# Kernel tuning notes

Measured on AMD Instinct MI355X. Metric: run time of the kernel, lower is better.

The kernel has to match this reference:

```python
import jax, jax.numpy as jnp
import numpy as np

EPS = 1e-5
SCALE = 30.0

def _ln(x, g, b):
    m = jnp.mean(x, axis=-1, keepdims=True)
    v = jnp.mean((x - m) ** 2, axis=-1, keepdims=True)
    return (x - m) * jax.lax.rsqrt(v + EPS) * g + b

def setup_inputs() -> dict:
    key = jax.random.key(0)
    ks = jax.random.split(key, 12)
    B, L, K, H, NIN = 4, 2048, 48, 128, 512
    s = 0.02
    return {
        "h_V": jax.random.normal(ks[0], (B, L, H), jnp.float32),
        "h_E": jax.random.normal(ks[1], (B, L, K, NIN - H), jnp.float32),
        "mask_V": jnp.ones((B, L), jnp.float32),
        "mask_E": jnp.ones((B, L, K), jnp.float32),
        "w1": jax.random.normal(ks[2], (NIN, H), jnp.float32) * s,
        "b1": jnp.zeros((H,), jnp.float32),
        "w2": jax.random.normal(ks[3], (H, H), jnp.float32) * s,
        "b2": jnp.zeros((H,), jnp.float32),
        "w3": jax.random.normal(ks[4], (H, H), jnp.float32) * s,
        "b3": jnp.zeros((H,), jnp.float32),
        "g1": jnp.ones((H,), jnp.float32),
        "bn1": jnp.zeros((H,), jnp.float32),
        "g2": jnp.ones((H,), jnp.float32),
        "bn2": jnp.zeros((H,), jnp.float32),
        "wf1": jax.random.normal(ks[5], (H, 4 * H), jnp.float32) * s,
        "bf1": jnp.zeros((4 * H,), jnp.float32),
        "wf2": jax.random.normal(ks[6], (4 * H, H), jnp.float32) * s,
        "bf2": jnp.zeros((H,), jnp.float32),
    }

def reference(h_V, h_E, mask_V, mask_E, w1, b1, w2, b2, w3, b3, g1, bn1, g2, bn2, wf1, bf1, wf2, bf2):
    B, L, H = h_V.shape
    K = h_E.shape[-2]
    gelu = lambda x: jax.nn.gelu(x, approximate=False)  # torch nn.GELU default (erf)
    # expand source node over K neighbors and concat: (B,L,K,num_in)
    h_V_exp = jnp.broadcast_to(h_V[:, :, None, :], (B, L, K, H))
    h_EV = jnp.concatenate([h_V_exp, h_E], axis=-1)
    h_msg = gelu(jnp.einsum('blki,ih->blkh', h_EV, w1) + b1)
    h_msg = gelu(jnp.einsum('blkh,hj->blkj', h_msg, w2) + b2)
    h_msg = jnp.einsum('blkh,hj->blkj', h_msg, w3) + b3
    h_msg = mask_E[..., None] * h_msg
    dh = jnp.sum(h_msg, axis=-2) / SCALE  # masked sum-aggregate over K
    h = _ln(h_V + dh, g1, bn1)
    dff = jnp.einsum('blh,hf->blf', h, wf1) + bf1
    dff = jnp.einsum('blf,fh->blh', gelu(dff), wf2) + bf2
    h = _ln(h + dff, g2, bn2)
    return mask_V[..., None] * h
```

## Files before the change

kernel.cpp:

```cpp
#include <hip/hip_runtime.h>
#include <hip/hip_bf16.h>


typedef __bf16 bf16x8 __attribute__((ext_vector_type(8)));
typedef __bf16 bf16x4 __attribute__((ext_vector_type(4)));
typedef float f32x4 __attribute__((ext_vector_type(4)));

#define HH 128
#define EE 384
#define KK 48

__device__ __forceinline__ float gelu_f(float x) {
  float x2 = x * x;
  float u = x * (-1.5957691216f - 0.0713548163f * x2);
  float e = __expf(u);
  return __fdividef(x, 1.0f + e);
}

__device__ __forceinline__ bf16x8 cvt8v(f32x4 a, f32x4 b) {
  bf16x8 r;
  #pragma unroll
  for (int i = 0; i < 4; ++i) { r[i] = (__bf16)a[i]; r[i + 4] = (__bf16)b[i]; }
  return r;
}

__device__ __forceinline__ f32x4 mfma16(bf16x8 a, bf16x8 b, f32x4 c) {
  return __builtin_amdgcn_mfma_f32_16x16x32_bf16(a, b, c, 0, 0, 0);
}

__device__ __forceinline__ void gload16(const void* g, void* l) {
  __builtin_amdgcn_global_load_lds(
      (const __attribute__((address_space(1))) void*)g,
      (__attribute__((address_space(3))) void*)l, 16, 0, 0);
}

__global__ void prep_kernel(const float* __restrict__ w1, const float* __restrict__ w2,
                            const float* __restrict__ w3, const float* __restrict__ wf1,
                            const float* __restrict__ wf2, __bf16* __restrict__ out) {
  int idx = blockIdx.x * 256 + threadIdx.x;
  if (idx < 49152) {
    int t = idx & 7, lane = (idx >> 3) & 63, n = (idx >> 9) & 7, kc = idx >> 12;
    int e = kc * 32 + (lane >> 4) * 8 + t, h = n * 16 + (lane & 15);
    out[idx] = (__bf16)w1[(128 + e) * 128 + h];
  } else if (idx < 65536) {
    int u = idx - 49152;
    int t = u & 7, lane = (u >> 3) & 63, n = (u >> 9) & 7, kc = u >> 12;
    int e = kc * 32 + (lane >> 4) * 8 + t, h = n * 16 + (lane & 15);
    out[idx] = (__bf16)w2[e * 128 + h];
  } else if (idx < 81920) {
    int u = idx - 65536;
    int t = u & 7, lane = (u >> 3) & 63, n = (u >> 9) & 7, kc = u >> 12;
    int e = kc * 32 + (lane >> 4) * 8 + t, h = n * 16 + (lane & 15);
    out[idx] = (__bf16)w3[e * 128 + h];
  } else if (idx < 147456) {
    int t = idx - 81920; int f = t >> 7, h = t & 127;
    out[idx] = (__bf16)wf1[h * 512 + f];
  } else if (idx < 212992) {
    int t = idx - 147456; int h = t >> 9, f = t & 511;
    out[idx] = (__bf16)wf2[f * 128 + h];
  }
}

__global__ __launch_bounds__(128) void v1_kernel(const float* __restrict__ hV,
                                                 const float* __restrict__ w1,
                                                 const float* __restrict__ b1,
                                                 float* __restrict__ V1) {
  __shared__ __align__(16) float sV[16][128];
  const int tid = threadIdx.x;
  const long p0 = (long)blockIdx.x * 16;
  for (int i = 0; i < 16; ++i) sV[i][tid] = hV[(p0 + i) * HH + tid];
  __syncthreads();
  float acc[16];
  float bb = b1[tid];
  #pragma unroll
  for (int p = 0; p < 16; ++p) acc[p] = bb;
  for (int k = 0; k < 128; k += 4) {
    float wa = w1[(k + 0) * HH + tid];
    float wb = w1[(k + 1) * HH + tid];
    float wc = w1[(k + 2) * HH + tid];
    float wd = w1[(k + 3) * HH + tid];
    #pragma unroll
    for (int p = 0; p < 16; ++p) {
      float4 h4 = *(const float4*)&sV[p][k];
      acc[p] = fmaf(h4.x, wa, fmaf(h4.y, wb, fmaf(h4.z, wc, fmaf(h4.w, wd, acc[p]))));
    }
  }
  #pragma unroll
  for (int p = 0; p < 16; ++p) V1[(p0 + p) * HH + tid] = acc[p];
}

__global__ __launch_bounds__(256, 2) void msg_kernel(
    const float* __restrict__ hE, const float* __restrict__ hV,
    const float* __restrict__ maskE,
    const __bf16* __restrict__ w1f, const __bf16* __restrict__ w2f,
    const __bf16* __restrict__ w3f, const float* __restrict__ V1,
    const float* __restrict__ b2, const float* __restrict__ b3,
    const float* __restrict__ g1, const float* __restrict__ bn1,
    float* __restrict__ outH) {
  __shared__ __align__(16) float sStage[4][4608];

  const int tid = threadIdx.x;
  const int lane = tid & 63;
  const int w = tid >> 6;
  const long p = (long)blockIdx.x * 4 + w;
  const int fr = lane & 15;
  const int fg = lane >> 4;
  char* stDst = (char*)&sStage[w][0];
  const int swz = (fr & 7) << 4;

  const int r_l = lane >> 3;
  const int cswz = ((lane & 7) ^ r_l) * 16;
  const char* gA = (const char*)(hE + p * KK * (long)EE) + r_l * (EE * 4) + cswz;

  const __bf16* b1p = w1f + lane * 8;
  const __bf16* b2p = w2f + lane * 8;
  const __bf16* b3p = w3f + lane * 8;

  f32x4 acc[3][8];
  #pragma unroll
  for (int m = 0; m < 3; ++m)
    #pragma unroll
    for (int n = 0; n < 8; ++n) acc[m][n] = (f32x4){0.f, 0.f, 0.f, 0.f};

  bf16x8 BsA[8], BsB[8];

#define STAGEA(KC, BUFI) { \
    _Pragma("unroll") for (int q_ = 0; q_ < 6; ++q_) \
      gload16(gA + (KC) * 128 + q_ * (8 * EE * 4), stDst + (BUFI) * 6144 + q_ * 1024); }
#define LOADB(BUF, BP, KC) { \
    _Pragma("unroll") for (int n_ = 0; n_ < 8; ++n_) \
      BUF[n_] = *(const bf16x8*)((BP) + ((KC) * 8 + n_) * 512); }
#define WAITV(N) asm volatile("s_waitcnt vmcnt(" #N ")" ::: "memory")

#define GITER(WAITN, BUFI, BUSE, DOSTAGE, STKC, STBUF, DOB, BLP, BLKC) { \
    WAITV(WAITN); \
    const char* rb_ = stDst + (BUFI) * 6144; \
    f32x4 x0_ = *(const f32x4*)(rb_ + fr * 128 + ((fg * 32) ^ swz)); \
    f32x4 x1_ = *(const f32x4*)(rb_ + fr * 128 + ((fg * 32 + 16) ^ swz)); \
    f32x4 x2_ = *(const f32x4*)(rb_ + (16 + fr) * 128 + ((fg * 32) ^ swz)); \
    f32x4 x3_ = *(const f32x4*)(rb_ + (16 + fr) * 128 + ((fg * 32 + 16) ^ swz)); \
    f32x4 x4_ = *(const f32x4*)(rb_ + (32 + fr) * 128 + ((fg * 32) ^ swz)); \
    f32x4 x5_ = *(const f32x4*)(rb_ + (32 + fr) * 128 + ((fg * 32 + 16) ^ swz)); \
    if (DOSTAGE) STAGEA(STKC, STBUF); \
    bf16x8 af0 = cvt8v(x0_, x1_); \
    bf16x8 af1 = cvt8v(x2_, x3_); \
    bf16x8 af2 = cvt8v(x4_, x5_); \
    _Pragma("unroll") for (int n_ = 0; n_ < 8; ++n_) { \
      acc[0][n_] = mfma16(BUSE[n_], af0, acc[0][n_]); \
      acc[1][n_] = mfma16(BUSE[n_], af1, acc[1][n_]); \
      acc[2][n_] = mfma16(BUSE[n_], af2, acc[2][n_]); } \
    if (DOB) LOADB(BUSE, BLP, BLKC); }

#define STEPL(BUSE, KC, DOB, BLP, BLKC) { \
    const int cb_ = (((KC) * 64 + fg * 16) ^ swz); \
    bf16x8 af0 = *(const bf16x8*)(stDst + fr * 256 + cb_); \
    bf16x8 af1 = *(const bf16x8*)(stDst + (16 + fr) * 256 + cb_); \
    bf16x8 af2 = *(const bf16x8*)(stDst + (32 + fr) * 256 + cb_); \
    _Pragma("unroll") for (int n_ = 0; n_ < 8; ++n_) { \
      acc[0][n_] = mfma16(BUSE[n_], af0, acc[0][n_]); \
      acc[1][n_] = mfma16(BUSE[n_], af1, acc[1][n_]); \
      acc[2][n_] = mfma16(BUSE[n_], af2, acc[2][n_]); } \
    if (DOB) LOADB(BUSE, BLP, BLKC); }

#define EPI(BIASQ) { \
    _Pragma("unroll") for (int m_ = 0; m_ < 3; ++m_) { \
      const int rb_ = (m_ * 16 + fr) * 256; \
      _Pragma("unroll") for (int n_ = 0; n_ < 8; ++n_) { \
        bf16x4 t_; \
        _Pragma("unroll") for (int j_ = 0; j_ < 4; ++j_) \
          t_[j_] = (__bf16)gelu_f(acc[m_][n_][j_] + BIASQ[n_][j_]); \
        *(bf16x4*)(stDst + rb_ + ((n_ * 32 + fg * 8) ^ swz)) = t_; \
        acc[m_][n_] = (f32x4){0.f, 0.f, 0.f, 0.f}; } } }

  STAGEA(0, 0);
  LOADB(BsA, b1p, 0);
  STAGEA(1, 1);
  LOADB(BsB, b1p, 1);

  GITER(14, 0, BsA, 1, 2, 2, 1, b1p, 2);
  GITER(14, 1, BsB, 1, 3, 0, 1, b1p, 3);
  GITER(14, 2, BsA, 1, 4, 1, 1, b1p, 4);
  GITER(14, 0, BsB, 1, 5, 2, 1, b1p, 5);
  GITER(14, 1, BsA, 1, 6, 0, 1, b1p, 6);
  GITER(14, 2, BsB, 1, 7, 1, 1, b1p, 7);
  GITER(14, 0, BsA, 1, 8, 2, 1, b1p, 8);
  GITER(14, 1, BsB, 1, 9, 0, 1, b1p, 9);
  GITER(14, 2, BsA, 1, 10, 1, 1, b1p, 10);
  GITER(14, 0, BsB, 1, 11, 2, 1, b1p, 11);

  f32x4 vq[8];
  #pragma unroll
  for (int n = 0; n < 8; ++n) vq[n] = *(const f32x4*)(V1 + p * HH + n * 16 + fg * 4);

  GITER(22, 1, BsA, 0, 0, 0, 1, b2p, 0);
  GITER(16, 2, BsB, 0, 0, 0, 1, b2p, 1);

  EPI(vq);

  { WAITV(8);  STEPL(BsA, 0, 1, b2p, 2); }
  { WAITV(8);  STEPL(BsB, 1, 1, b2p, 3); }
  { WAITV(8);  STEPL(BsA, 2, 1, b3p, 0); }
  { WAITV(8);  STEPL(BsB, 3, 1, b3p, 1); }
  {
    f32x4 bq[8];
    #pragma unroll
    for (int n = 0; n < 8; ++n) bq[n] = *(const f32x4*)(b2 + n * 16 + fg * 4);
    EPI(bq);
  }

  { STEPL(BsA, 0, 1, b3p, 2); }
  { STEPL(BsB, 1, 1, b3p, 3); }
  { WAITV(8);  STEPL(BsA, 2, 0, b3p, 0); }
  { WAITV(0);  STEPL(BsB, 3, 0, b3p, 0); }

  const float mk0 = maskE[p * KK + fr];
  const float mk1 = maskE[p * KK + 16 + fr];
  const float mk2 = maskE[p * KK + 32 + fr];
  f32x4 red[8];
  {
    #pragma unroll
    for (int n = 0; n < 8; ++n) {
      f32x4 bq = *(const f32x4*)(b3 + n * 16 + fg * 4);
      red[n] = mk0 * (acc[0][n] + bq) + mk1 * (acc[1][n] + bq) + mk2 * (acc[2][n] + bq);
    }
    #pragma unroll
    for (int off = 1; off <= 8; off <<= 1)
      #pragma unroll
      for (int n = 0; n < 8; ++n)
        #pragma unroll
        for (int j = 0; j < 4; ++j)
          red[n][j] += __shfl_xor(red[n][j], off);
  }

  {
    f32x4 xq[8];
    #pragma unroll
    for (int n = 0; n < 8; ++n)
      xq[n] = *(const f32x4*)(hV + p * HH + n * 16 + fg * 4) + red[n] * (1.f / 30.f);
    float s = 0.f;
    #pragma unroll
    for (int n = 0; n < 8; ++n)
      #pragma unroll
      for (int j = 0; j < 4; ++j) s += xq[n][j];
    s += __shfl_xor(s, 16); s += __shfl_xor(s, 32);
    float mean = s * (1.f / 128.f);
    float qv = 0.f;
    #pragma unroll
    for (int n = 0; n < 8; ++n)
      #pragma unroll
      for (int j = 0; j < 4; ++j) { float e = xq[n][j] - mean; qv += e * e; }
    qv += __shfl_xor(qv, 16); qv += __shfl_xor(qv, 32);
    float rs = rsqrtf(qv * (1.f / 128.f) + 1e-5f);
    if (fr == 0) {
      #pragma unroll
      for (int n = 0; n < 8; ++n) {
        f32x4 gq = *(const f32x4*)(g1 + n * 16 + fg * 4);
        f32x4 bq = *(const f32x4*)(bn1 + n * 16 + fg * 4);
        f32x4 o;
        #pragma unroll
        for (int j = 0; j < 4; ++j) o[j] = (xq[n][j] - mean) * rs * gq[j] + bq[j];
        *(f32x4*)(outH + p * HH + n * 16 + fg * 4) = o;
      }
    }
  }
#undef STAGEA
#undef LOADB
#undef WAITV
#undef GITER
#undef STEPL
#undef EPI
}

__global__ __launch_bounds__(256, 2) void ffn_kernel(
    const float* __restrict__ xin, const __bf16* __restrict__ wf1t,
    const float* __restrict__ bf1, const __bf16* __restrict__ wf2t,
    const float* __restrict__ bf2, const float* __restrict__ g2,
    const float* __restrict__ bn2, const float* __restrict__ maskV,
    float* __restrict__ out) {
  __shared__ __align__(16) __bf16 sX[32][136];
  __shared__ __align__(16) __bf16 sH1[32][520];
  __shared__ __align__(16) float sOut[32][132];
  const int tid = threadIdx.x, lane = tid & 63, w = tid >> 6;
  const long row0 = (long)blockIdx.x * 32;
  const int fr = lane & 15, fg = lane >> 4;

  {
    int r = tid >> 3, c = (tid & 7) * 16;
    const float* src = xin + (row0 + r) * HH + c;
    f32x4 v0 = *(const f32x4*)src, v1 = *(const f32x4*)(src + 4);
    f32x4 v2 = *(const f32x4*)(src + 8), v3 = *(const f32x4*)(src + 12);
    *(bf16x8*)&sX[r][c] = cvt8v(v0, v1);
    *(bf16x8*)&sX[r][c + 8] = cvt8v(v2, v3);
  }
  __syncthreads();

  f32x4 a1[2][8];
  #pragma unroll
  for (int m = 0; m < 2; ++m)
    #pragma unroll
    for (int n = 0; n < 8; ++n) a1[m][n] = (f32x4){0.f, 0.f, 0.f, 0.f};
  for (int kc = 0; kc < 4; ++kc) {
    int k0 = kc * 32;
    bf16x8 af0 = *(const bf16x8*)&sX[fr][k0 + fg * 8];
    bf16x8 af1 = *(const bf16x8*)&sX[16 + fr][k0 + fg * 8];
    #pragma unroll
    for (int n = 0; n < 8; ++n) {
      const __bf16* bp = wf1t + (long)(w * 128 + n * 16 + fr) * HH + k0 + fg * 8;
      bf16x8 bfr = *(const bf16x8*)bp;
      a1[0][n] = mfma16(af0, bfr, a1[0][n]);
      a1[1][n] = mfma16(af1, bfr, a1[1][n]);
    }
  }
  #pragma unroll
  for (int n = 0; n < 8; ++n) {
    float bv = bf1[w * 128 + n * 16 + fr];
    #pragma unroll
    for (int m = 0; m < 2; ++m)
      #pragma unroll
      for (int j = 0; j < 4; ++j)
        sH1[m * 16 + fg * 4 + j][w * 128 + n * 16 + fr] = (__bf16)gelu_f(a1[m][n][j] + bv);
  }
  __syncthreads();

  f32x4 a2[2][2];
  #pragma unroll
  for (int m = 0; m < 2; ++m)
    #pragma unroll
    for (int n = 0; n < 2; ++n) a2[m][n] = (f32x4){0.f, 0.f, 0.f, 0.f};
  for (int kc = 0; kc < 16; ++kc) {
    int k0 = kc * 32;
    bf16x8 af0 = *(const bf16x8*)&sH1[fr][k0 + fg * 8];
    bf16x8 af1 = *(const bf16x8*)&sH1[16 + fr][k0 + fg * 8];
    #pragma unroll
    for (int n = 0; n < 2; ++n) {
      const __bf16* bp = wf2t + (long)(w * 32 + n * 16 + fr) * 512 + k0 + fg * 8;
      bf16x8 bfr = *(const bf16x8*)bp;
      a2[0][n] = mfma16(af0, bfr, a2[0][n]);
      a2[1][n] = mfma16(af1, bfr, a2[1][n]);
    }
  }
  #pragma unroll
  for (int n = 0; n < 2; ++n) {
    float bv = bf2[w * 32 + n * 16 + fr];
    #pragma unroll
    for (int m = 0; m < 2; ++m)
      #pragma unroll
      for (int j = 0; j < 4; ++j)
        sOut[m * 16 + fg * 4 + j][w * 32 + n * 16 + fr] = a2[m][n][j] + bv;
  }
  __syncthreads();

  {
    int r = tid >> 3, c0 = (tid & 7) * 16;
    long p = row0 + r;
    const float* xp = xin + p * HH + c0;
    float x[16];
    #pragma unroll
    for (int i = 0; i < 16; ++i) x[i] = xp[i] + sOut[r][c0 + i];
    float s = 0.f;
    #pragma unroll
    for (int i = 0; i < 16; ++i) s += x[i];
    s += __shfl_xor(s, 1); s += __shfl_xor(s, 2); s += __shfl_xor(s, 4);
    float mean = s * (1.f / 128.f);
    float q = 0.f;
    #pragma unroll
    for (int i = 0; i < 16; ++i) { float e = x[i] - mean; q += e * e; }
    q += __shfl_xor(q, 1); q += __shfl_xor(q, 2); q += __shfl_xor(q, 4);
    float rs = rsqrtf(q * (1.f / 128.f) + 1e-5f);
    float mv = maskV[p];
    float* op = out + p * HH + c0;
    #pragma unroll
    for (int i = 0; i < 16; ++i)
      op[i] = ((x[i] - mean) * rs * g2[c0 + i] + bn2[c0 + i]) * mv;
  }
}

extern "C" void kernel_launch(void* const* d_in, const int* in_sizes, int n_in,
                              void* d_out, int out_size, void* d_ws, size_t ws_size,
                              hipStream_t stream) {
  const float* hV    = (const float*)d_in[0];
  const float* hE    = (const float*)d_in[1];
  const float* maskV = (const float*)d_in[2];
  const float* maskE = (const float*)d_in[3];
  const float* w1    = (const float*)d_in[4];
  const float* b1    = (const float*)d_in[5];
  const float* w2    = (const float*)d_in[6];
  const float* b2    = (const float*)d_in[7];
  const float* w3    = (const float*)d_in[8];
  const float* b3    = (const float*)d_in[9];
  const float* g1    = (const float*)d_in[10];
  const float* bn1   = (const float*)d_in[11];
  const float* g2    = (const float*)d_in[12];
  const float* bn2   = (const float*)d_in[13];
  const float* wf1   = (const float*)d_in[14];
  const float* bf1   = (const float*)d_in[15];
  const float* wf2   = (const float*)d_in[16];
  const float* bf2   = (const float*)d_in[17];
  float* out = (float*)d_out;

  __bf16* wsb = (__bf16*)d_ws;
  float* V1   = (float*)((char*)d_ws + 425984);
  float* hbuf = (float*)((char*)d_ws + 4620288);

  prep_kernel<<<832, 256, 0, stream>>>(w1, w2, w3, wf1, wf2, wsb);
  v1_kernel<<<512, 128, 0, stream>>>(hV, w1, b1, V1);
  msg_kernel<<<2048, 256, 0, stream>>>(hE, hV, maskE,
                                       wsb, wsb + 49152, wsb + 65536, V1,
                                       b2, b3, g1, bn1, hbuf);
  ffn_kernel<<<256, 256, 0, stream>>>(hbuf, wsb + 81920, bf1, wsb + 147456, bf2,
                                      g2, bn2, maskV, out);
}
```

Baseline: 211.9 us.

## Process two nodes per wave in msg_kernel with cross-node prefetch pipelining

Each wave now handles two nodes instead of one, and the grid is halved. The first h_E chunks of the second node are prefetched into LDS during the first node's layer-2/3 work, so the second node's load latency hides behind compute. V1 and hV rows are staged into LDS through async global_load_lds, and the bias and LayerNorm parameters are cached in shared memory once per block. In exchange the kernel gets much more complex vmcnt accounting, uses more LDS per block, and launches half as many blocks, which gives fewer of them to spread across the GPU.

```diff
diff --git a/kernel.cpp b/kernel.cpp
--- a/kernel.cpp
+++ b/kernel.cpp
@@ -32,6 +32,11 @@
   __builtin_amdgcn_global_load_lds(
       (const __attribute__((address_space(1))) void*)g,
       (__attribute__((address_space(3))) void*)l, 16, 0, 0);
+}
+__device__ __forceinline__ void gload4(const void* g, void* l) {
+  __builtin_amdgcn_global_load_lds(
+      (const __attribute__((address_space(1))) void*)g,
+      (__attribute__((address_space(3))) void*)l, 4, 0, 0);
 }
 
 __global__ void prep_kernel(const float* __restrict__ w1, const float* __restrict__ w2,
@@ -98,24 +103,43 @@
     const float* __restrict__ g1, const float* __restrict__ bn1,
     float* __restrict__ outH) {
   __shared__ __align__(16) float sStage[4][4608];
+  __shared__ __align__(16) float sAux[4][256];
+  __shared__ __align__(16) float sBias[512];
 
   const int tid = threadIdx.x;
   const int lane = tid & 63;
   const int w = tid >> 6;
-  const long p = (long)blockIdx.x * 4 + w;
   const int fr = lane & 15;
   const int fg = lane >> 4;
+
+  for (int j = tid; j < 512; j += 256) {
+    float v;
+    if (j < 128) v = b2[j];
+    else if (j < 256) v = b3[j - 128];
+    else if (j < 384) v = g1[j - 256];
+    else v = bn1[j - 384];
+    sBias[j] = v;
+  }
+  __syncthreads();
+
+  const long p0 = (long)blockIdx.x * 8 + w * 2;
+  const long p1 = p0 + 1;
   char* stDst = (char*)&sStage[w][0];
+  char* auxDst = (char*)&sAux[w][0];
+  const char* biasB = (const char*)&sBias[0];
   const int swz = (fr & 7) << 4;
-
   const int r_l = lane >> 3;
   const int cswz = ((lane & 7) ^ r_l) * 16;
-  const char* gA = (const char*)(hE + p * KK * (long)EE) + r_l * (EE * 4) + cswz;
+  const char* gA0 = (const char*)(hE + p0 * KK * (long)EE) + r_l * (EE * 4) + cswz;
+  const char* gA1 = gA0 + (long)KK * EE * 4;
 
   const __bf16* b1p = w1f + lane * 8;
   const __bf16* b2p = w2f + lane * 8;
   const __bf16* b3p = w3f + lane * 8;
 
+  const float mkA0 = maskE[p0 * KK + fr], mkA1 = maskE[p0 * KK + 16 + fr], mkA2 = maskE[p0 * KK + 32 + fr];
+  const float mkB0 = maskE[p1 * KK + fr], mkB1 = maskE[p1 * KK + 16 + fr], mkB2 = maskE[p1 * KK + 32 + fr];
+
   f32x4 acc[3][8];
   #pragma unroll
   for (int m = 0; m < 3; ++m)
@@ -124,16 +148,21 @@
 
   bf16x8 BsA[8], BsB[8];
 
-#define STAGEA(KC, BUFI) { \
+#define STAGEA(GB, KC, BUFI) { \
     _Pragma("unroll") for (int q_ = 0; q_ < 6; ++q_) \
-      gload16(gA + (KC) * 128 + q_ * (8 * EE * 4), stDst + (BUFI) * 6144 + q_ * 1024); }
+      gload16((GB) + (KC) * 128 + q_ * (8 * EE * 4), stDst + (BUFI) * 6144 + q_ * 1024); }
+#define STAGEAUX(PP) { \
+    gload4(V1 + (PP) * HH + lane, auxDst); \
+    gload4(V1 + (PP) * HH + 64 + lane, auxDst + 256); \
+    gload4(hV + (PP) * HH + lane, auxDst + 512); \
+    gload4(hV + (PP) * HH + 64 + lane, auxDst + 768); }
 #define LOADB(BUF, BP, KC) { \
     _Pragma("unroll") for (int n_ = 0; n_ < 8; ++n_) \
       BUF[n_] = *(const bf16x8*)((BP) + ((KC) * 8 + n_) * 512); }
 #define WAITV(N) asm volatile("s_waitcnt vmcnt(" #N ")" ::: "memory")
 
-#define GITER(WAITN, BUFI, BUSE, DOSTAGE, STKC, STBUF, DOB, BLP, BLKC) { \
-    WAITV(WAITN); \
+#define GITER(WN, BUFI, BUSE, DOSTAGE, GB, STKC, STBUF, BLP, BLKC) { \
+    WAITV(WN); \
     const char* rb_ = stDst + (BUFI) * 6144; \
     f32x4 x0_ = *(const f32x4*)(rb_ + fr * 128 + ((fg * 32) ^ swz)); \
     f32x4 x1_ = *(const f32x4*)(rb_ + fr * 128 + ((fg * 32 + 16) ^ swz)); \
@@ -141,7 +170,7 @@
     f32x4 x3_ = *(const f32x4*)(rb_ + (16 + fr) * 128 + ((fg * 32 + 16) ^ swz)); \
     f32x4 x4_ = *(const f32x4*)(rb_ + (32 + fr) * 128 + ((fg * 32) ^ swz)); \
     f32x4 x5_ = *(const f32x4*)(rb_ + (32 + fr) * 128 + ((fg * 32 + 16) ^ swz)); \
-    if (DOSTAGE) STAGEA(STKC, STBUF); \
+    if (DOSTAGE) STAGEA(GB, STKC, STBUF); \
     bf16x8 af0 = cvt8v(x0_, x1_); \
     bf16x8 af1 = cvt8v(x2_, x3_); \
     bf16x8 af2 = cvt8v(x4_, x5_); \
@@ -149,9 +178,10 @@
       acc[0][n_] = mfma16(BUSE[n_], af0, acc[0][n_]); \
       acc[1][n_] = mfma16(BUSE[n_], af1, acc[1][n_]); \
       acc[2][n_] = mfma16(BUSE[n_], af2, acc[2][n_]); } \
-    if (DOB) LOADB(BUSE, BLP, BLKC); }
-
-#define STEPL(BUSE, KC, DOB, BLP, BLKC) { \
+    LOADB(BUSE, BLP, BLKC); }
+
+#define STEPL(WN, BUSE, KC, DOB, BLP, BLKC) { \
+    WAITV(WN); \
     const int cb_ = (((KC) * 64 + fg * 16) ^ swz); \
     bf16x8 af0 = *(const bf16x8*)(stDst + fr * 256 + cb_); \
     bf16x8 af1 = *(const bf16x8*)(stDst + (16 + fr) * 256 + cb_); \
@@ -162,113 +192,146 @@
       acc[2][n_] = mfma16(BUSE[n_], af2, acc[2][n_]); } \
     if (DOB) LOADB(BUSE, BLP, BLKC); }
 
-#define EPI(BIASQ) { \
+#define EPICORE(BQ) { \
     _Pragma("unroll") for (int m_ = 0; m_ < 3; ++m_) { \
       const int rb_ = (m_ * 16 + fr) * 256; \
       _Pragma("unroll") for (int n_ = 0; n_ < 8; ++n_) { \
         bf16x4 t_; \
         _Pragma("unroll") for (int j_ = 0; j_ < 4; ++j_) \
-          t_[j_] = (__bf16)gelu_f(acc[m_][n_][j_] + BIASQ[n_][j_]); \
+          t_[j_] = (__bf16)gelu_f(acc[m_][n_][j_] + BQ[n_][j_]); \
         *(bf16x4*)(stDst + rb_ + ((n_ * 32 + fg * 8) ^ swz)) = t_; \
         acc[m_][n_] = (f32x4){0.f, 0.f, 0.f, 0.f}; } } }
 
-  STAGEA(0, 0);
+#define REDLN(M0, M1, M2, PP) { \
+    f32x4 red[8]; \
+    _Pragma("unroll") for (int n_ = 0; n_ < 8; ++n_) { \
+      f32x4 bq_ = *(const f32x4*)(biasB + (128 + n_ * 16 + fg * 4) * 4); \
+      red[n_] = (M0) * (acc[0][n_] + bq_) + (M1) * (acc[1][n_] + bq_) + (M2) * (acc[2][n_] + bq_); \
+      acc[0][n_] = (f32x4){0.f, 0.f, 0.f, 0.f}; \
+      acc[1][n_] = (f32x4){0.f, 0.f, 0.f, 0.f}; \
+      acc[2][n_] = (f32x4){0.f, 0.f, 0.f, 0.f}; } \
+    _Pragma("unroll") for (int off_ = 1; off_ <= 8; off_ <<= 1) \
+      _Pragma("unroll") for (int n_ = 0; n_ < 8; ++n_) \
+        _Pragma("unroll") for (int j_ = 0; j_ < 4; ++j_) \
+          red[n_][j_] += __shfl_xor(red[n_][j_], off_); \
+    f32x4 xq[8]; \
+    _Pragma("unroll") for (int n_ = 0; n_ < 8; ++n_) { \
+      f32x4 hq_ = *(const f32x4*)(auxDst + 512 + (n_ * 16 + fg * 4) * 4); \
+      xq[n_] = hq_ + red[n_] * (1.f / 30.f); } \
+    float s_ = 0.f; \
+    _Pragma("unroll") for (int n_ = 0; n_ < 8; ++n_) \
+      _Pragma("unroll") for (int j_ = 0; j_ < 4; ++j_) s_ += xq[n_][j_]; \
+    s_ += __shfl_xor(s_, 16); s_ += __shfl_xor(s_, 32); \
+    float mean_ = s_ * (1.f / 128.f); \
+    float qv_ = 0.f; \
+    _Pragma("unroll") for (int n_ = 0; n_ < 8; ++n_) \
+      _Pragma("unroll") for (int j_ = 0; j_ < 4; ++j_) { float e_ = xq[n_][j_] - mean_; qv_ += e_ * e_; } \
+    qv_ += __shfl_xor(qv_, 16); qv_ += __shfl_xor(qv_, 32); \
+    float rs_ = rsqrtf(qv_ * (1.f / 128.f) + 1e-5f); \
+    if (fr == 0) { \
+      _Pragma("unroll") for (int n_ = 0; n_ < 8; ++n_) { \
+        f32x4 gq_ = *(const f32x4*)(biasB + (256 + n_ * 16 + fg * 4) * 4); \
+        f32x4 bq_ = *(const f32x4*)(biasB + (384 + n_ * 16 + fg * 4) * 4); \
+        f32x4 o_; \
+        _Pragma("unroll") for (int j_ = 0; j_ < 4; ++j_) \
+          o_[j_] = (xq[n_][j_] - mean_) * rs_ * gq_[j_] + bq_[j_]; \
+        *(f32x4*)(outH + (PP) * HH + n_ * 16 + fg * 4) = o_; } } }
+
+  STAGEA(gA0, 0, 0);
   LOADB(BsA, b1p, 0);
-  STAGEA(1, 1);
+  STAGEA(gA0, 1, 1);
   LOADB(BsB, b1p, 1);
 
-  GITER(14, 0, BsA, 1, 2, 2, 1, b1p, 2);
-  GITER(14, 1, BsB, 1, 3, 0, 1, b1p, 3);
-  GITER(14, 2, BsA, 1, 4, 1, 1, b1p, 4);
-  GITER(14, 0, BsB, 1, 5, 2, 1, b1p, 5);
-  GITER(14, 1, BsA, 1, 6, 0, 1, b1p, 6);
-  GITER(14, 2, BsB, 1, 7, 1, 1, b1p, 7);
-  GITER(14, 0, BsA, 1, 8, 2, 1, b1p, 8);
-  GITER(14, 1, BsB, 1, 9, 0, 1, b1p, 9);
-  GITER(14, 2, BsA, 1, 10, 1, 1, b1p, 10);
-  GITER(14, 0, BsB, 1, 11, 2, 1, b1p, 11);
-
-  f32x4 vq[8];
-  #pragma unroll
-  for (int n = 0; n < 8; ++n) vq[n] = *(const f32x4*)(V1 + p * HH + n * 16 + fg * 4);
-
-  GITER(22, 1, BsA, 0, 0, 0, 1, b2p, 0);
-  GITER(16, 2, BsB, 0, 0, 0, 1, b2p, 1);
-
-  EPI(vq);
-
-  { WAITV(8);  STEPL(BsA, 0, 1, b2p, 2); }
-  { WAITV(8);  STEPL(BsB, 1, 1, b2p, 3); }
-  { WAITV(8);  STEPL(BsA, 2, 1, b3p, 0); }
-  { WAITV(8);  STEPL(BsB, 3, 1, b3p, 1); }
+  GITER(14, 0, BsA, 1, gA0, 2, 2, b1p, 2);
+  GITER(14, 1, BsB, 1, gA0, 3, 0, b1p, 3);
+  GITER(14, 2, BsA, 1, gA0, 4, 1, b1p, 4);
+  GITER(14, 0, BsB, 1, gA0, 5, 2, b1p, 5);
+  GITER(14, 1, BsA, 1, gA0, 6, 0, b1p, 6);
+  GITER(14, 2, BsB, 1, gA0, 7, 1, b1p, 7);
+  GITER(14, 0, BsA, 1, gA0, 8, 2, b1p, 8);
+  GITER(14, 1, BsB, 1, gA0, 9, 0, b1p, 9);
+  GITER(14, 2, BsA, 1, gA0, 10, 1, b1p, 10);
+  GITER(14, 0, BsB, 1, gA0, 11, 2, b1p, 11);
+  STAGEAUX(p0);
+  GITER(18, 1, BsA, 0, gA0, 0, 0, b2p, 0);
+  GITER(12, 2, BsB, 0, gA0, 0, 0, b2p, 1);
+
+  WAITV(18);
+  {
+    f32x4 vq[8];
+    #pragma unroll
+    for (int n = 0; n < 8; ++n) vq[n] = *(const f32x4*)(auxDst + (n * 16 + fg * 4) * 4);
+    STAGEA(gA1, 0, 2);
+    EPICORE(vq);
+  }
+
+  STEPL(14, BsA, 0, 1, b2p, 2);
+  STEPL(14, BsB, 1, 1, b2p, 3);
+  STEPL(8,  BsA, 2, 1, b3p, 0);
+  STEPL(8,  BsB, 3, 1, b3p, 1);
   {
     f32x4 bq[8];
     #pragma unroll
-    for (int n = 0; n < 8; ++n) bq[n] = *(const f32x4*)(b2 + n * 16 + fg * 4);
-    EPI(bq);
-  }
-
-  { STEPL(BsA, 0, 1, b3p, 2); }
-  { STEPL(BsB, 1, 1, b3p, 3); }
-  { WAITV(8);  STEPL(BsA, 2, 0, b3p, 0); }
-  { WAITV(0);  STEPL(BsB, 3, 0, b3p, 0); }
-
-  const float mk0 = maskE[p * KK + fr];
-  const float mk1 = maskE[p * KK + 16 + fr];
-  const float mk2 = maskE[p * KK + 32 + fr];
-  f32x4 red[8];
-  {
-    #pragma unroll
-    for (int n = 0; n < 8; ++n) {
-      f32x4 bq = *(const f32x4*)(b3 + n * 16 + fg * 4);
-      red[n] = mk0 * (acc[0][n] + bq) + mk1 * (acc[1][n] + bq) + mk2 * (acc[2][n] + bq);
-    }
-    #pragma unroll
-    for (int off = 1; off <= 8; off <<= 1)
-      #pragma unroll
-      for (int n = 0; n < 8; ++n)
-        #pragma unroll
-        for (int j = 0; j < 4; ++j)
-          red[n][j] += __shfl_xor(red[n][j], off);
-  }
-
-  {
-    f32x4 xq[8];
-    #pragma unroll
-    for (int n = 0; n < 8; ++n)
-      xq[n] = *(const f32x4*)(hV + p * HH + n * 16 + fg * 4) + red[n] * (1.f / 30.f);
-    float s = 0.f;
-    #pragma unroll
-    for (int n = 0; n < 8; ++n)
-      #pragma unroll
-      for (int j = 0; j < 4; ++j) s += xq[n][j];
-    s += __shfl_xor(s, 16); s += __shfl_xor(s, 32);
-    float mean = s * (1.f / 128.f);
-    float qv = 0.f;
-    #pragma unroll
-    for (int n = 0; n < 8; ++n)
-      #pragma unroll
-      for (int j = 0; j < 4; ++j) { float e = xq[n][j] - mean; qv += e * e; }
-    qv += __shfl_xor(qv, 16); qv += __shfl_xor(qv, 32);
-    float rs = rsqrtf(qv * (1.f / 128.f) + 1e-5f);
-    if (fr == 0) {
-      #pragma unroll
-      for (int n = 0; n < 8; ++n) {
-        f32x4 gq = *(const f32x4*)(g1 + n * 16 + fg * 4);
-        f32x4 bq = *(const f32x4*)(bn1 + n * 16 + fg * 4);
-        f32x4 o;
-        #pragma unroll
-        for (int j = 0; j < 4; ++j) o[j] = (xq[n][j] - mean) * rs * gq[j] + bq[j];
-        *(f32x4*)(outH + p * HH + n * 16 + fg * 4) = o;
-      }
-    }
-  }
+    for (int n = 0; n < 8; ++n) bq[n] = *(const f32x4*)(biasB + (n * 16 + fg * 4) * 4);
+    EPICORE(bq);
+  }
+
+  STEPL(8, BsA, 0, 1, b3p, 2);
+  STEPL(8, BsB, 1, 1, b3p, 3);
+  STEPL(8, BsA, 2, 1, b1p, 0);
+  STEPL(8, BsB, 3, 1, b1p, 1);
+  STAGEA(gA1, 1, 0);
+
+  REDLN(mkA0, mkA1, mkA2, p0);
+
+  GITER(22, 2, BsA, 1, gA1, 2, 1, b1p, 2);
+  GITER(22, 0, BsB, 1, gA1, 3, 2, b1p, 3);
+  GITER(14, 1, BsA, 1, gA1, 4, 0, b1p, 4);
+  GITER(14, 2, BsB, 1, gA1, 5, 1, b1p, 5);
+  GITER(14, 0, BsA, 1, gA1, 6, 2, b1p, 6);
+  GITER(14, 1, BsB, 1, gA1, 7, 0, b1p, 7);
+  GITER(14, 2, BsA, 1, gA1, 8, 1, b1p, 8);
+  GITER(14, 0, BsB, 1, gA1, 9, 2, b1p, 9);
+  GITER(14, 1, BsA, 1, gA1, 10, 0, b1p, 10);
+  GITER(14, 2, BsB, 1, gA1, 11, 1, b1p, 11);
+  STAGEAUX(p1);
+  GITER(18, 0, BsA, 0, gA1, 0, 0, b2p, 0);
+  GITER(12, 1, BsB, 0, gA1, 0, 0, b2p, 1);
+
+  WAITV(18);
+  {
+    f32x4 vq[8];
+    #pragma unroll
+    for (int n = 0; n < 8; ++n) vq[n] = *(const f32x4*)(auxDst + (n * 16 + fg * 4) * 4);
+    EPICORE(vq);
+  }
+
+  STEPL(8, BsA, 0, 1, b2p, 2);
+  STEPL(8, BsB, 1, 1, b2p, 3);
+  STEPL(8, BsA, 2, 1, b3p, 0);
+  STEPL(8, BsB, 3, 1, b3p, 1);
+  {
+    f32x4 bq[8];
+    #pragma unroll
+    for (int n = 0; n < 8; ++n) bq[n] = *(const f32x4*)(biasB + (n * 16 + fg * 4) * 4);
+    EPICORE(bq);
+  }
+
+  STEPL(8, BsA, 0, 1, b3p, 2);
+  STEPL(8, BsB, 1, 1, b3p, 3);
+  STEPL(8, BsA, 2, 0, b3p, 0);
+  STEPL(0, BsB, 3, 0, b3p, 0);
+
+  REDLN(mkB0, mkB1, mkB2, p1);
+
 #undef STAGEA
+#undef STAGEAUX
 #undef LOADB
 #undef WAITV
 #undef GITER
 #undef STEPL
-#undef EPI
+#undef EPICORE
+#undef REDLN
 }
 
 __global__ __launch_bounds__(256, 2) void ffn_kernel(
@@ -404,7 +467,7 @@
 
   prep_kernel<<<832, 256, 0, stream>>>(w1, w2, w3, wf1, wf2, wsb);
   v1_kernel<<<512, 128, 0, stream>>>(hV, w1, b1, V1);
-  msg_kernel<<<2048, 256, 0, stream>>>(hE, hV, maskE,
+  msg_kernel<<<1024, 256, 0, stream>>>(hE, hV, maskE,
                                        wsb, wsb + 49152, wsb + 65536, V1,
                                        b2, b3, g1, bn1, hbuf);
   ffn_kernel<<<256, 256, 0, stream>>>(hbuf, wsb + 81920, bf1, wsb + 147456, bf2,
```

Result: slower. 546.4 us (+157.8%).
